# Performance work log

Hardware: AMD Instinct MI355X
Metric: run time of the kernel (lower is better)

The kernel has to match this reference:

```python
import jax, jax.numpy as jnp
import numpy as np

NUM_CLASSES = 200
NUM_FEATURES = 128
NUM_PROTO_PER_CLASS = 10
NUM_PROTOTYPES = NUM_CLASSES * NUM_PROTO_PER_CLASS
EPS = 1e-4
INCORRECT_STRENGTH = -0.5


def _make_last_layer_weight():
    # prototype_class_identity[j, j // num_proto_per_class] = 1; weight = correct + (-0.5)*incorrect
    proto_ids = np.arange(NUM_PROTOTYPES) // NUM_PROTO_PER_CLASS  # (P,)
    correct = (np.arange(NUM_CLASSES)[:, None] == proto_ids[None, :]).astype(np.float32)  # (C, P)
    weight = correct + INCORRECT_STRENGTH * (1.0 - correct)
    return jnp.asarray(weight)


def setup_inputs() -> dict:
    key = jax.random.key(0)
    k1, k2 = jax.random.split(key)
    features = jax.random.normal(k1, (64, NUM_FEATURES, 14, 14), dtype=jnp.float32)
    # SHIFTED_NORMAL prototype init: small-variance normal shifted by 0.5
    prototypes = 0.5 + 0.1 * jax.random.normal(k2, (NUM_PROTOTYPES, NUM_FEATURES, 1, 1), dtype=jnp.float32)
    last_weight = _make_last_layer_weight()  # (C, P)
    return {"features": features, "prototypes": prototypes, "last_weight": last_weight}


def reference(features, prototypes, last_weight):
    # features: (N, D, H, W); prototypes: (P, D, 1, 1); last_weight: (C, P)
    protos = prototypes[:, :, 0, 0]  # (P, D)
    x_sq = jnp.sum(features * features, axis=1, keepdims=True)  # (N, 1, H, W)
    p_sq = jnp.sum(protos * protos, axis=1)  # (P,)
    xp = jnp.einsum("ndhw,pd->nphw", features, protos)  # (N, P, H, W)
    dist = jax.nn.relu(x_sq + p_sq[None, :, None, None] - 2.0 * xp)  # (N, P, H, W)
    sim = jnp.log((dist + 1.0) / (dist + EPS))  # (N, P, H, W)
    sim_max = jnp.max(sim.reshape(sim.shape[0], sim.shape[1], -1), axis=2)  # (N, P)
    logits = sim_max @ last_weight.T  # (N, C)
    min_dist = jnp.min(dist.reshape(dist.shape[0], dist.shape[1], -1), axis=2)  # (N, P)
    return (logits, min_dist)
```

## Files before the change

### kernel.cpp

```cpp
#include <hip/hip_runtime.h>
#include <hip/hip_bf16.h>

#define NUM_CLASSES 200
#define NF 128
#define NP 2000
#define NPC 10
#define HW 196
#define MPAD 208
#define NB 64
#define EPSV 1e-4f
#define PTILE 250
#define CTILE 25

typedef __attribute__((ext_vector_type(8))) short short8;
typedef __attribute__((ext_vector_type(4))) float f32x4;

static __device__ __forceinline__ unsigned short f2bf(float x) {
    __hip_bfloat16 h = __float2bfloat16(x);
    return __builtin_bit_cast(unsigned short, h);
}

__global__ __launch_bounds__(256, 2) void kmain(const float* __restrict__ f,
                                                const float* __restrict__ protos,
                                                const float* __restrict__ W,
                                                float* __restrict__ min_out,
                                                float* __restrict__ logits) {
    __shared__ unsigned short sf[MPAD * NF];
    __shared__ float swp[13 * 4 * 4 * 4];
    __shared__ float sxsq[MPAD];
    __shared__ float scsum[32];
    float* const ssim = (float*)sf;

    const int n    = blockIdx.x;
    const int pt   = blockIdx.y;
    const int t    = threadIdx.x;
    const int wave = t >> 6;
    const int lane = t & 63;
    const int row  = lane & 15;
    const int quad = lane >> 4;
    const int sb   = wave * 64;
    const int p0   = pt * PTILE;

    const int kb  = t >> 2;
    const int hwl = (t & 3) * 4;
    const int u0  = kb >> 3;
    const int klo = kb & 7;
    const float* fb0 = f + ((size_t)n * NF + kb) * HW + hwl;
    const float* fb1 = fb0 + (size_t)64 * HW;

    #pragma unroll
    for (int mt = 0; mt < 13; ++mt) {
        const int hw0 = mt * 16;
        float4 v0 = make_float4(0.f, 0.f, 0.f, 0.f), v1 = v0;
        if (hw0 + hwl + 4 <= HW) {
            v0 = *(const float4*)(fb0 + hw0);
            v1 = *(const float4*)(fb1 + hw0);
        }
        float4 sq;
        sq.x = v0.x * v0.x + v1.x * v1.x;
        sq.y = v0.y * v0.y + v1.y * v1.y;
        sq.z = v0.z * v0.z + v1.z * v1.z;
        sq.w = v0.w * v0.w + v1.w * v1.w;
        #pragma unroll
        for (int off = 4; off <= 32; off <<= 1) {
            sq.x += __shfl_xor(sq.x, off, 64);
            sq.y += __shfl_xor(sq.y, off, 64);
            sq.z += __shfl_xor(sq.z, off, 64);
            sq.w += __shfl_xor(sq.w, off, 64);
        }
        if (lane < 4) *(float4*)&swp[(mt * 16 + wave * 4 + lane) * 4] = sq;

        const float a0[4] = {v0.x, v0.y, v0.z, v0.w};
        const float a1[4] = {v1.x, v1.y, v1.z, v1.w};
        #pragma unroll
        for (int j = 0; j < 4; ++j) {
            const int hw  = hw0 + hwl + j;
            const int idx = hw * 128 + ((u0 ^ (hw & 15)) << 3) + klo;
            sf[idx]      = f2bf(a0[j]);
            sf[idx ^ 64] = f2bf(a1[j]);
        }
    }

    short8 A[4][4];
    float psum[4];
    #pragma unroll
    for (int g = 0; g < 4; ++g) {
        int p = p0 + sb + g * 16 + row;
        const float* ap = protos + (size_t)(p < NP ? p : NP - 1) * NF + quad * 8;
        psum[g] = 0.f;
        #pragma unroll
        for (int kk = 0; kk < 4; ++kk) {
            float4 w0 = *(const float4*)(ap + kk * 32);
            float4 w1 = *(const float4*)(ap + kk * 32 + 4);
            psum[g] += w0.x * w0.x + w0.y * w0.y + w0.z * w0.z + w0.w * w0.w
                     + w1.x * w1.x + w1.y * w1.y + w1.z * w1.z + w1.w * w1.w;
            short8 a;
            a[0] = (short)f2bf(w0.x); a[1] = (short)f2bf(w0.y);
            a[2] = (short)f2bf(w0.z); a[3] = (short)f2bf(w0.w);
            a[4] = (short)f2bf(w1.x); a[5] = (short)f2bf(w1.y);
            a[6] = (short)f2bf(w1.z); a[7] = (short)f2bf(w1.w);
            A[g][kk] = a;
        }
        psum[g] += __shfl_xor(psum[g], 16, 64);
        psum[g] += __shfl_xor(psum[g], 32, 64);
    }

    __syncthreads();

    if (t < MPAD) {
        const int mt = t >> 4;
        const int cj = t & 15;
        float s = swp[(mt * 16 +  0 + cj >> 0) * 0];
        s = swp[(mt * 16 +  0) * 4 + 0];
        s = swp[(mt * 16 + 0 * 4) * 4];
        const int c = cj >> 2, j = cj & 3;
        s = swp[(mt * 16 + 0 * 4 + c) * 4 + j]
          + swp[(mt * 16 + 1 * 4 + c) * 4 + j]
          + swp[(mt * 16 + 2 * 4 + c) * 4 + j]
          + swp[(mt * 16 + 3 * 4 + c) * 4 + j];
        sxsq[t] = (t < HW) ? s : 3.0e38f;
    }
    __syncthreads();

    float runmin[4][4];
    #pragma unroll
    for (int g = 0; g < 4; ++g)
        #pragma unroll
        for (int r = 0; r < 4; ++r) runmin[g][r] = 3.0e38f;

    const short8* sfv = (const short8*)sf;
    for (int mt = 0; mt < 13; ++mt) {
        const int base = (mt * 16 + row) * 16;
        short8 b0 = sfv[base + ((quad + 0)  ^ row)];
        short8 b1 = sfv[base + ((quad + 4)  ^ row)];
        short8 b2 = sfv[base + ((quad + 8)  ^ row)];
        short8 b3 = sfv[base + ((quad + 12) ^ row)];
        float xv = sxsq[mt * 16 + row];

        #pragma unroll
        for (int g = 0; g < 4; ++g) {
            f32x4 acc = {0.f, 0.f, 0.f, 0.f};
            acc = __builtin_amdgcn_mfma_f32_16x16x32_bf16(A[g][0], b0, acc, 0, 0, 0);
            acc = __builtin_amdgcn_mfma_f32_16x16x32_bf16(A[g][1], b1, acc, 0, 0, 0);
            acc = __builtin_amdgcn_mfma_f32_16x16x32_bf16(A[g][2], b2, acc, 0, 0, 0);
            acc = __builtin_amdgcn_mfma_f32_16x16x32_bf16(A[g][3], b3, acc, 0, 0, 0);
            #pragma unroll
            for (int r = 0; r < 4; ++r)
                runmin[g][r] = fminf(runmin[g][r], xv - 2.f * acc[r]);
        }
    }

    __syncthreads();

    #pragma unroll
    for (int g = 0; g < 4; ++g) {
        #pragma unroll
        for (int off = 1; off < 16; off <<= 1)
            #pragma unroll
            for (int r = 0; r < 4; ++r)
                runmin[g][r] = fminf(runmin[g][r], __shfl_xor(runmin[g][r], off, 64));
        #pragma unroll
        for (int r = 0; r < 4; ++r) {
            float psq_sel = __shfl(psum[g], 20 * quad + r, 64);
            int slot = sb + g * 16 + quad * 4 + r;
            if (row == 0) {
                float sim = 0.f;
                if (slot < PTILE) {
                    float m = fmaxf(runmin[g][r] + psq_sel, 0.f);
                    min_out[(size_t)n * NP + p0 + slot] = m;
                    sim = logf((m + 1.f) / (m + EPSV));
                }
                ssim[slot] = sim;
            }
        }
    }
    __syncthreads();

    if (t < CTILE) {
        float s = 0.f;
        #pragma unroll
        for (int j = 0; j < NPC; ++j) s += ssim[t * NPC + j];
        scsum[t] = s;
    }
    __syncthreads();

    if (t < NUM_CLASSES) {
        const float a = W[0];
        const float b = W[NPC];
        float tp = 0.f;
        #pragma unroll
        for (int j = 0; j < CTILE; ++j) tp += scsum[j];
        float v = b * tp;
        const int c0 = pt * CTILE;
        if (t >= c0 && t < c0 + CTILE) v += (a - b) * scsum[t - c0];
        atomicAdd(&logits[(size_t)n * NUM_CLASSES + t], v);
    }
}

extern "C" void kernel_launch(void* const* d_in, const int* in_sizes, int n_in,
                              void* d_out, int out_size, void* d_ws, size_t ws_size,
                              hipStream_t stream) {
    const float* f      = (const float*)d_in[0];
    const float* protos = (const float*)d_in[1];
    const float* W      = (const float*)d_in[2];

    float* logits   = (float*)d_out;
    float* min_dist = (float*)d_out + NB * NUM_CLASSES;

    (void)d_ws; (void)ws_size;

    hipMemsetAsync(logits, 0, (size_t)NB * NUM_CLASSES * sizeof(float), stream);
    kmain<<<dim3(NB, 8), 256, 0, stream>>>(f, protos, W, min_dist, logits);
}
```

Before: 82.55 us.

## Double block size to 500 prototypes and stage features through a transposed LDS tile

Each block now runs 512 threads and handles 500 prototypes, so the grid shrinks to 64x4 and each sample's features are loaded and converted half as many times. Feature staging changes from direct scattered 2-byte LDS stores to a padded fp32 transpose tile. From that tile each thread reads a column, computes the squared norm and writes a 16-byte bf16 vector. This cuts redundant global feature reads and the narrow LDS writes. In exchange it adds more barriers per round and halves the block count (256 blocks), which may lower parallelism on a large GPU.

```diff
diff --git a/kernel.cpp b/kernel.cpp
--- a/kernel.cpp
+++ b/kernel.cpp
@@ -7,10 +7,12 @@
 #define NPC 10
 #define HW 196
 #define MPAD 208
+#define NCH 13
 #define NB 64
 #define EPSV 1e-4f
-#define PTILE 250
-#define CTILE 25
+#define TROW 17
+#define PTILE 500
+#define CTILE 50
 
 typedef __attribute__((ext_vector_type(8))) short short8;
 typedef __attribute__((ext_vector_type(4))) float f32x4;
@@ -20,15 +22,15 @@
     return __builtin_bit_cast(unsigned short, h);
 }
 
-__global__ __launch_bounds__(256, 2) void kmain(const float* __restrict__ f,
+__global__ __launch_bounds__(512, 2) void kmain(const float* __restrict__ f,
                                                 const float* __restrict__ protos,
                                                 const float* __restrict__ W,
                                                 float* __restrict__ min_out,
                                                 float* __restrict__ logits) {
     __shared__ unsigned short sf[MPAD * NF];
-    __shared__ float swp[13 * 4 * 4 * 4];
+    __shared__ float tile[2][NF * TROW];
     __shared__ float sxsq[MPAD];
-    __shared__ float scsum[32];
+    __shared__ float scsum[64];
     float* const ssim = (float*)sf;
 
     const int n    = blockIdx.x;
@@ -40,46 +42,6 @@
     const int quad = lane >> 4;
     const int sb   = wave * 64;
     const int p0   = pt * PTILE;
-
-    const int kb  = t >> 2;
-    const int hwl = (t & 3) * 4;
-    const int u0  = kb >> 3;
-    const int klo = kb & 7;
-    const float* fb0 = f + ((size_t)n * NF + kb) * HW + hwl;
-    const float* fb1 = fb0 + (size_t)64 * HW;
-
-    #pragma unroll
-    for (int mt = 0; mt < 13; ++mt) {
-        const int hw0 = mt * 16;
-        float4 v0 = make_float4(0.f, 0.f, 0.f, 0.f), v1 = v0;
-        if (hw0 + hwl + 4 <= HW) {
-            v0 = *(const float4*)(fb0 + hw0);
-            v1 = *(const float4*)(fb1 + hw0);
-        }
-        float4 sq;
-        sq.x = v0.x * v0.x + v1.x * v1.x;
-        sq.y = v0.y * v0.y + v1.y * v1.y;
-        sq.z = v0.z * v0.z + v1.z * v1.z;
-        sq.w = v0.w * v0.w + v1.w * v1.w;
-        #pragma unroll
-        for (int off = 4; off <= 32; off <<= 1) {
-            sq.x += __shfl_xor(sq.x, off, 64);
-            sq.y += __shfl_xor(sq.y, off, 64);
-            sq.z += __shfl_xor(sq.z, off, 64);
-            sq.w += __shfl_xor(sq.w, off, 64);
-        }
-        if (lane < 4) *(float4*)&swp[(mt * 16 + wave * 4 + lane) * 4] = sq;
-
-        const float a0[4] = {v0.x, v0.y, v0.z, v0.w};
-        const float a1[4] = {v1.x, v1.y, v1.z, v1.w};
-        #pragma unroll
-        for (int j = 0; j < 4; ++j) {
-            const int hw  = hw0 + hwl + j;
-            const int idx = hw * 128 + ((u0 ^ (hw & 15)) << 3) + klo;
-            sf[idx]      = f2bf(a0[j]);
-            sf[idx ^ 64] = f2bf(a1[j]);
-        }
-    }
 
     short8 A[4][4];
     float psum[4];
@@ -105,20 +67,49 @@
         psum[g] += __shfl_xor(psum[g], 32, 64);
     }
 
-    __syncthreads();
-
-    if (t < MPAD) {
-        const int mt = t >> 4;
-        const int cj = t & 15;
-        float s = swp[(mt * 16 +  0 + cj >> 0) * 0];
-        s = swp[(mt * 16 +  0) * 4 + 0];
-        s = swp[(mt * 16 + 0 * 4) * 4];
-        const int c = cj >> 2, j = cj & 3;
-        s = swp[(mt * 16 + 0 * 4 + c) * 4 + j]
-          + swp[(mt * 16 + 1 * 4 + c) * 4 + j]
-          + swp[(mt * 16 + 2 * 4 + c) * 4 + j]
-          + swp[(mt * 16 + 3 * 4 + c) * 4 + j];
-        sxsq[t] = (t < HW) ? s : 3.0e38f;
+    const int tl   = t & 255;
+    const int ch   = t >> 8;
+    const int kb   = tl >> 2;
+    const int hwl  = (tl & 3) * 4;
+    const int hwl2 = tl >> 4;
+    const int kg   = tl & 15;
+
+    for (int rd = 0; rd < 7; ++rd) {
+        const int mt  = rd * 2 + ch;
+        const int hw0 = mt * 16;
+        float4 v0 = make_float4(0.f, 0.f, 0.f, 0.f), v1 = v0;
+        if (mt < NCH && hw0 + hwl + 4 <= HW) {
+            v0 = *(const float4*)(f + ((size_t)n * NF + kb) * HW + hw0 + hwl);
+            v1 = *(const float4*)(f + ((size_t)n * NF + kb + 64) * HW + hw0 + hwl);
+        }
+        __syncthreads();
+        if (mt < NCH) {
+            tile[ch][kb * TROW + hwl + 0] = v0.x;
+            tile[ch][kb * TROW + hwl + 1] = v0.y;
+            tile[ch][kb * TROW + hwl + 2] = v0.z;
+            tile[ch][kb * TROW + hwl + 3] = v0.w;
+            tile[ch][(kb + 64) * TROW + hwl + 0] = v1.x;
+            tile[ch][(kb + 64) * TROW + hwl + 1] = v1.y;
+            tile[ch][(kb + 64) * TROW + hwl + 2] = v1.z;
+            tile[ch][(kb + 64) * TROW + hwl + 3] = v1.w;
+        }
+        __syncthreads();
+        if (mt < NCH) {
+            float xp = 0.f;
+            unsigned short u[8];
+            #pragma unroll
+            for (int j = 0; j < 8; ++j) {
+                float val = tile[ch][(kg * 8 + j) * TROW + hwl2];
+                xp += val * val;
+                u[j] = f2bf(val);
+            }
+            ((uint4*)sf)[(hw0 + hwl2) * 16 + (kg ^ hwl2)] = *(uint4*)u;
+            xp += __shfl_xor(xp, 1, 64);
+            xp += __shfl_xor(xp, 2, 64);
+            xp += __shfl_xor(xp, 4, 64);
+            xp += __shfl_xor(xp, 8, 64);
+            if (kg == 0) sxsq[hw0 + hwl2] = (hw0 + hwl2 < HW) ? xp : 3.0e38f;
+        }
     }
     __syncthreads();
 
@@ -129,7 +120,7 @@
         for (int r = 0; r < 4; ++r) runmin[g][r] = 3.0e38f;
 
     const short8* sfv = (const short8*)sf;
-    for (int mt = 0; mt < 13; ++mt) {
+    for (int mt = 0; mt < NCH; ++mt) {
         const int base = (mt * 16 + row) * 16;
         short8 b0 = sfv[base + ((quad + 0)  ^ row)];
         short8 b1 = sfv[base + ((quad + 4)  ^ row)];
@@ -210,5 +201,5 @@
     (void)d_ws; (void)ws_size;
 
     hipMemsetAsync(logits, 0, (size_t)NB * NUM_CLASSES * sizeof(float), stream);
-    kmain<<<dim3(NB, 8), 256, 0, stream>>>(f, protos, W, min_dist, logits);
+    kmain<<<dim3(NB, 4), 512, 0, stream>>>(f, protos, W, min_dist, logits);
 }
```

Result: no change. 82.48 us (-0.1%).
